# Kernel tuning notes

Hardware: AMD Instinct MI355X
Metric: run time of the kernel (lower is better)

Reference implementation:

```python
import jax, jax.numpy as jnp
import numpy as np

D_MODEL = 1024
N_HEADS = 16
HEAD_DIM = D_MODEL // N_HEADS
B, S = 2, 2048


def setup_inputs() -> dict:
    key = jax.random.key(0)
    ks = jax.random.split(key, 10)
    sd = 1.0 / np.sqrt(D_MODEL)
    return {
        "x": jax.random.normal(ks[0], (B, S, D_MODEL), dtype=jnp.float32),
        "mask": jnp.ones((1, 1, S, S), dtype=jnp.int32),
        "Wq": jax.random.normal(ks[1], (D_MODEL, D_MODEL), dtype=jnp.float32) * sd,
        "bq": jax.random.normal(ks[2], (D_MODEL,), dtype=jnp.float32) * sd,
        "Wk": jax.random.normal(ks[3], (D_MODEL, D_MODEL), dtype=jnp.float32) * sd,
        "bk": jax.random.normal(ks[4], (D_MODEL,), dtype=jnp.float32) * sd,
        "Wv": jax.random.normal(ks[5], (D_MODEL, D_MODEL), dtype=jnp.float32) * sd,
        "bv": jax.random.normal(ks[6], (D_MODEL,), dtype=jnp.float32) * sd,
        "Wo": jax.random.normal(ks[7], (D_MODEL, D_MODEL), dtype=jnp.float32) * sd,
        "bo": jax.random.normal(ks[8], (D_MODEL,), dtype=jnp.float32) * sd,
    }


def reference(x, mask, Wq, bq, Wk, bk, Wv, bv, Wo, bo):
    b, s, _ = x.shape
    scale = HEAD_DIM ** -0.5
    # projections (torch Linear: x @ W.T + b); split heads -> [b, h, s, d]
    def split_heads(t):
        return t.reshape(b, s, N_HEADS, HEAD_DIM).transpose(0, 2, 1, 3)
    q = split_heads(x @ Wq.T + bq)
    k = split_heads(x @ Wk.T + bk)
    v = split_heads(x @ Wv.T + bv)
    # scores: [b, h, s, s]
    scores = jnp.einsum("bhqd,bhkd->bhqk", q, k) * scale
    scores = jnp.where(mask == 0, jnp.float32(-1e20), scores)
    probs = jax.nn.softmax(scores, axis=-1)
    # dropout_rate = 0.0 (eval): identity
    ctx = jnp.einsum("bhqk,bhkd->bhqd", probs, v)
    ctx = ctx.transpose(0, 2, 1, 3).reshape(b, s, D_MODEL)
    return ctx @ Wo.T + bo
```

## Files before the change

### kernel.cpp

```cpp
#include <hip/hip_runtime.h>
#include <hip/hip_bf16.h>
#include <cstdint>
#include <cstddef>

#define D_MODEL 1024
#define NH      16
#define HD      64
#define BATCH   2
#define SEQ     2048
#define MTOT    (BATCH*SEQ)

typedef __bf16 bf16;
typedef __attribute__((ext_vector_type(8)))  __bf16 bf16x8;
typedef __attribute__((ext_vector_type(4)))  __bf16 bf16x4;
typedef __attribute__((ext_vector_type(2)))  __bf16 bf16x2;
typedef __attribute__((ext_vector_type(4)))  float  f32x4;
typedef __attribute__((ext_vector_type(16))) float  f32x16;
typedef __attribute__((ext_vector_type(2)))  unsigned int uint32x2;

__device__ __forceinline__ void gl_lds16(const void* g, void* l) {
    __builtin_amdgcn_global_load_lds(
        (const __attribute__((address_space(1))) uint32_t*)g,
        (__attribute__((address_space(3))) uint32_t*)l, 16, 0, 0);
}

__device__ __forceinline__ uint32_t pkbf(float a, float b) {
    union { bf16x2 v; uint32_t u; } t;
    t.v = (bf16x2){ (bf16)a, (bf16)b };
    return t.u;
}

__global__ __launch_bounds__(256)
void convert_all(const float* __restrict__ x,
                 const float* __restrict__ Wq, const float* __restrict__ Wk,
                 const float* __restrict__ Wv, const float* __restrict__ Wo,
                 bf16* __restrict__ xb,
                 bf16* __restrict__ Wqb, bf16* __restrict__ Wkb,
                 bf16* __restrict__ Wvb, bf16* __restrict__ Wob)
{
    const float* src; bf16* dst; size_t base = 0;
    int y = blockIdx.y;
    if      (y < 4)  { src = x;  dst = xb;  base = (size_t)y << 20; }
    else if (y == 4) { src = Wq; dst = Wqb; }
    else if (y == 5) { src = Wk; dst = Wkb; }
    else if (y == 6) { src = Wv; dst = Wvb; }
    else             { src = Wo; dst = Wob; }
    size_t i = base + ((size_t)blockIdx.x * 256 + threadIdx.x) * 4;
    float4 v = *(const float4*)(src + i);
    bf16x4 o = { (bf16)v.x, (bf16)v.y, (bf16)v.z, (bf16)v.w };
    *(bf16x4*)(dst + i) = o;
}

template<int MODE, int NTN>
__device__ __forceinline__ void gemm_body(const bf16* __restrict__ A,
                                          const bf16* __restrict__ W,
                                          const float* __restrict__ bias,
                                          void* __restrict__ OutV,
                                          float oscale, int mBase, int nBase,
                                          bf16* As, bf16* Bs)
{
    const int t      = threadIdx.x;
    const int l      = t & 63;
    const int w      = t >> 6;
    const int lane15 = l & 15;
    const int quad   = l >> 4;
    const int wm     = w >> 1;
    const int wn     = w & 1;
    const int WN     = NTN * 16;

    const int colsw = (((t & 7) ^ ((t >> 3) & 7))) * 16;
    const int sw    = lane15 & 7;

    const f32x4 vzero = {0.0f, 0.0f, 0.0f, 0.0f};
    f32x4 acc[4][NTN];
#pragma unroll
    for (int mt = 0; mt < 4; ++mt)
#pragma unroll
        for (int nt = 0; nt < NTN; ++nt) acc[mt][nt] = vzero;

    float bn_[NTN];
    float bm_[4][4];
    if (MODE == 3) {
#pragma unroll
        for (int mt = 0; mt < 4; ++mt)
#pragma unroll
            for (int r = 0; r < 4; ++r)
                bm_[mt][r] = bias[mBase + wm*64 + mt*16 + quad*4 + r];
    } else {
#pragma unroll
        for (int nt = 0; nt < NTN; ++nt)
            bn_[nt] = bias[nBase + wn*WN + nt*16 + lane15];
    }

    auto stage = [&](int kk, int buf) {
        char* Ad = (char*)As + buf * 16384;
        char* Bd = (char*)Bs + buf * (NTN * 4096);
#pragma unroll
        for (int c = 0; c < 4; ++c) {
            int row = (c*256 + t) >> 3;
            gl_lds16((const char*)A + (size_t)(mBase + row)*2048 + kk*2 + colsw,
                     Ad + (c*256 + w*64)*16);
        }
#pragma unroll
        for (int c = 0; c < NTN; ++c) {
            int row = (c*256 + t) >> 3;
            gl_lds16((const char*)W + (size_t)(nBase + row)*2048 + kk*2 + colsw,
                     Bd + (c*256 + w*64)*16);
        }
    };

    stage(0, 0);
    __syncthreads();
    stage(64, 1);

    for (int kt = 0; kt < 16; ++kt) {
        const int cb = kt & 1;
        const bf16* Ab = As + cb * 8192;
        const bf16* Bb = Bs + cb * (NTN * 2048);

#pragma unroll
        for (int kc = 0; kc < 2; ++kc) {
            bf16x8 af[4], bfr[NTN];
#pragma unroll
            for (int mt = 0; mt < 4; ++mt)
                af[mt] = *(const bf16x8*)(Ab + (wm*64 + mt*16 + lane15)*64
                                             + (((kc*4 + quad) ^ sw) * 8));
#pragma unroll
            for (int nt = 0; nt < NTN; ++nt)
                bfr[nt] = *(const bf16x8*)(Bb + (wn*WN + nt*16 + lane15)*64
                                              + (((kc*4 + quad) ^ sw) * 8));
#pragma unroll
            for (int mt = 0; mt < 4; ++mt)
#pragma unroll
                for (int nt = 0; nt < NTN; ++nt)
                    acc[mt][nt] = __builtin_amdgcn_mfma_f32_16x16x32_bf16(
                        af[mt], bfr[nt], acc[mt][nt], 0, 0, 0);
        }

        if (kt < 15) {
            __syncthreads();
            if (kt < 14) stage((kt + 2) * 64, cb);
        }
    }

#pragma unroll
    for (int mt = 0; mt < 4; ++mt) {
#pragma unroll
        for (int nt = 0; nt < NTN; ++nt) {
            int o = nBase + wn*WN + nt*16 + lane15;
#pragma unroll
            for (int r = 0; r < 4; ++r) {
                int m = mBase + wm*64 + mt*16 + quad*4 + r;
                if (MODE == 0) {
                    ((float*)OutV)[(size_t)m*D_MODEL + o] =
                        (acc[mt][nt][r] + bn_[nt]) * oscale;
                } else if (MODE == 1) {
                    int b = m >> 11, s = m & (SEQ-1);
                    int h = o >> 6,  dd = o & (HD-1);
                    ((bf16*)OutV)[(((size_t)(b*NH + h))*SEQ + s)*HD + dd] =
                        (bf16)((acc[mt][nt][r] + bn_[nt]) * oscale);
                } else {
                    int b = o >> 11, s = o & (SEQ-1);
                    int h = m >> 6,  dd = m & (HD-1);
                    ((bf16*)OutV)[(((size_t)(b*NH + h))*HD + dd)*SEQ + s] =
                        (bf16)((acc[mt][nt][r] + bm_[mt][r]) * oscale);
                }
            }
        }
    }
}

#define QSCALE (0.125f * 1.44269504088896f)

__global__ __launch_bounds__(256)
void gemm_qkv(const bf16* __restrict__ X,
              const bf16* __restrict__ Wq, const float* __restrict__ bq,
              const bf16* __restrict__ Wk, const float* __restrict__ bk,
              const bf16* __restrict__ Wv, const float* __restrict__ bv,
              bf16* __restrict__ Q, bf16* __restrict__ K, bf16* __restrict__ Vt)
{
    __shared__ __align__(16) bf16 As[2*128*64];
    __shared__ __align__(16) bf16 Bs[2*128*64];
    int lin = blockIdx.x + 8*blockIdx.y + 256*blockIdx.z;
    int wl  = (lin & 7)*96 + (lin >> 3);
    int bx = wl & 7, by = (wl >> 3) & 31, bz = wl >> 8;
    if (bz == 0)
        gemm_body<1,4>(X, Wq, bq, Q, QSCALE, by*128, bx*128, As, Bs);
    else if (bz == 1)
        gemm_body<1,4>(X, Wk, bk, K, 1.0f, by*128, bx*128, As, Bs);
    else
        gemm_body<3,4>(Wv, X, bv, Vt, 1.0f, bx*128, by*128, As, Bs);
}

__global__ __launch_bounds__(256)
void gemm_out(const bf16* __restrict__ A, const bf16* __restrict__ W,
              const float* __restrict__ b, float* __restrict__ O)
{
    __shared__ __align__(16) bf16 As[2*128*64];
    __shared__ __align__(16) bf16 Bs[2*64*64];
    int lin = blockIdx.x + 16*blockIdx.y;
    int wl  = (lin & 7)*64 + (lin >> 3);
    int bx = wl & 15, by = wl >> 4;
    gemm_body<0,2>(A, W, b, O, 1.0f, by*128, bx*64, As, Bs);
}

__device__ __forceinline__ float expsum(f32x16& s0, f32x16& s1) {
    float ps[4] = {0.f, 0.f, 0.f, 0.f};
#pragma unroll
    for (int e = 0; e < 16; ++e) {
        float p0 = __builtin_amdgcn_exp2f(s0[e]); s0[e] = p0;
        float p1 = __builtin_amdgcn_exp2f(s1[e]); s1[e] = p1;
        ps[e & 3] += p0 + p1;
    }
    return (ps[0] + ps[1]) + (ps[2] + ps[3]);
}

__device__ __forceinline__ void build_pf(const f32x16& s0, const f32x16& s1,
                                         bf16x8* pf) {
    uint32_t pp[8], pq[8];
#pragma unroll
    for (int i = 0; i < 8; ++i) {
        pp[i] = pkbf(s0[2*i], s0[2*i+1]);
        pq[i] = pkbf(s1[2*i], s1[2*i+1]);
    }
    union { uint32_t u[4]; bf16x8 f; } fr;
    uint32x2 r0, r1;
    r0 = __builtin_amdgcn_permlane32_swap(pp[0], pp[2], false, false);
    r1 = __builtin_amdgcn_permlane32_swap(pp[1], pp[3], false, false);
    fr.u[0] = r0[0]; fr.u[1] = r1[0]; fr.u[2] = r0[1]; fr.u[3] = r1[1];
    pf[0] = fr.f;
    r0 = __builtin_amdgcn_permlane32_swap(pp[4], pp[6], false, false);
    r1 = __builtin_amdgcn_permlane32_swap(pp[5], pp[7], false, false);
    fr.u[0] = r0[0]; fr.u[1] = r1[0]; fr.u[2] = r0[1]; fr.u[3] = r1[1];
    pf[1] = fr.f;
    r0 = __builtin_amdgcn_permlane32_swap(pq[0], pq[2], false, false);
    r1 = __builtin_amdgcn_permlane32_swap(pq[1], pq[3], false, false);
    fr.u[0] = r0[0]; fr.u[1] = r1[0]; fr.u[2] = r0[1]; fr.u[3] = r1[1];
    pf[2] = fr.f;
    r0 = __builtin_amdgcn_permlane32_swap(pq[4], pq[6], false, false);
    r1 = __builtin_amdgcn_permlane32_swap(pq[5], pq[7], false, false);
    fr.u[0] = r0[0]; fr.u[1] = r1[0]; fr.u[2] = r0[1]; fr.u[3] = r1[1];
    pf[3] = fr.f;
}

__global__ __launch_bounds__(512, 2)
void attn(const bf16* __restrict__ Qg, const bf16* __restrict__ Kg,
          const bf16* __restrict__ Vtg, bf16* __restrict__ ctx)
{
    __shared__ __align__(16) bf16 SMEM[2*16384];

    const int t      = threadIdx.x;
    const int w      = t >> 6;
    const int wg     = w >> 2;
    const int wq     = w & 3;
    const int l      = t & 63;
    const int lane31 = l & 31;
    const int half   = l >> 5;

    int lin = blockIdx.x + 8*blockIdx.y + 128*blockIdx.z;
    int wl  = (lin & 7)*32 + (lin >> 3);
    const int qt = wl & 7;
    const int h  = (wl >> 3) & 15;
    const int b  = wl >> 7;
    const size_t bh = (size_t)(b*NH + h);
    const bf16* Qb  = Qg  + bh*SEQ*HD;
    const bf16* Kb  = Kg  + bh*SEQ*HD;
    const bf16* Vtb = Vtg + bh*HD*SEQ;

    const int qA = qt*256 + wq*32 + lane31;

    bf16x8 qfA[4], qfB[4];
#pragma unroll
    for (int kc = 0; kc < 4; ++kc) {
        qfA[kc] = *(const bf16x8*)(Qb + (size_t)qA*HD + kc*16 + half*8);
        qfB[kc] = *(const bf16x8*)(Qb + (size_t)(qA+128)*HD + kc*16 + half*8);
    }

    const int lrow = l >> 3;
    const int csw  = ((l & 7) ^ lrow) * 8;

    auto issue = [&](int it, int buf) {
        const int kb = it * 128;
        bf16* Kbase = SMEM + buf*16384;
        bf16* Vbase = SMEM + buf*16384 + 8192;
#pragma unroll
        for (int seg = 0; seg < 2; ++seg) {
            int Rb = w*16 + seg*8;
            int R  = Rb + lrow;
            gl_lds16(Kb + (size_t)(kb + R)*HD + csw, Kbase + Rb*64);
            gl_lds16(Vtb + (size_t)(R & 63)*SEQ + kb + ((R >> 6) << 6) + csw,
                     Vbase + Rb*64);
        }
    };

    issue(0, 0);
    __syncthreads();
    issue(1, 1);

    float lA = 0.0f, lB = 0.0f;
    f32x16 oA0 = (f32x16)0.0f, oA1 = (f32x16)0.0f;
    f32x16 oB0 = (f32x16)0.0f, oB1 = (f32x16)0.0f;

    const int swl = lane31 & 7;
    const int NT2 = SEQ / 128;
    for (int kt = 0; kt < NT2; ++kt) {
        const int cb = kt & 1;
        const bf16* KsB = SMEM + cb*16384 + wg*64*64;
        const bf16* VsB = SMEM + cb*16384 + 8192 + wg*64*64;

        f32x16 sA0 = (f32x16)0.0f, sA1 = (f32x16)0.0f;
        f32x16 sB0 = (f32x16)0.0f, sB1 = (f32x16)0.0f;
#pragma unroll
        for (int kc = 0; kc < 4; ++kc) {
            const int co = ((kc*2 + half) ^ swl) * 8;
            bf16x8 k0 = *(const bf16x8*)(KsB + lane31*64      + co);
            bf16x8 k1 = *(const bf16x8*)(KsB + (32+lane31)*64 + co);
            sA0 = __builtin_amdgcn_mfma_f32_32x32x16_bf16(k0, qfA[kc], sA0, 0, 0, 0);
            sA1 = __builtin_amdgcn_mfma_f32_32x32x16_bf16(k1, qfA[kc], sA1, 0, 0, 0);
            sB0 = __builtin_amdgcn_mfma_f32_32x32x16_bf16(k0, qfB[kc], sB0, 0, 0, 0);
            sB1 = __builtin_amdgcn_mfma_f32_32x32x16_bf16(k1, qfB[kc], sB1, 0, 0, 0);
        }

        lA += expsum(sA0, sA1);
        bf16x8 pfA[4];
        build_pf(sA0, sA1, pfA);
        lB += expsum(sB0, sB1);
        bf16x8 pfB[4];
        build_pf(sB0, sB1, pfB);

#pragma unroll
        for (int kk = 0; kk < 4; ++kk) {
            const int co = ((kk*2 + half) ^ swl) * 8;
            bf16x8 v0 = *(const bf16x8*)(VsB + lane31*64      + co);
            bf16x8 v1 = *(const bf16x8*)(VsB + (32+lane31)*64 + co);
            oA0 = __builtin_amdgcn_mfma_f32_32x32x16_bf16(v0, pfA[kk], oA0, 0, 0, 0);
            oA1 = __builtin_amdgcn_mfma_f32_32x32x16_bf16(v1, pfA[kk], oA1, 0, 0, 0);
            oB0 = __builtin_amdgcn_mfma_f32_32x32x16_bf16(v0, pfB[kk], oB0, 0, 0, 0);
            oB1 = __builtin_amdgcn_mfma_f32_32x32x16_bf16(v1, pfB[kk], oB1, 0, 0, 0);
        }

        if (kt < NT2-1) {
            __syncthreads();
            if (kt + 2 < NT2) issue(kt + 2, cb);
        }
    }

    {
        union { float f; uint32_t u; } c; c.f = lA;
        uint32x2 r = __builtin_amdgcn_permlane32_swap(c.u, c.u, false, false);
        union { uint32_t u; float f; } x0, x1; x0.u = r[0]; x1.u = r[1];
        lA = x0.f + x1.f;
        c.f = lB;
        r = __builtin_amdgcn_permlane32_swap(c.u, c.u, false, false);
        x0.u = r[0]; x1.u = r[1];
        lB = x0.f + x1.f;
    }

    __syncthreads();
    float* sc = (float*)SMEM;
    const int sidx = (wq*64 + l)*36;
    if (wg == 1) {
        *(f32x4*)(sc + sidx +  0) = (f32x4){oA0[0],oA0[1],oA0[2],oA0[3]};
        *(f32x4*)(sc + sidx +  4) = (f32x4){oA0[4],oA0[5],oA0[6],oA0[7]};
        *(f32x4*)(sc + sidx +  8) = (f32x4){oA0[8],oA0[9],oA0[10],oA0[11]};
        *(f32x4*)(sc + sidx + 12) = (f32x4){oA0[12],oA0[13],oA0[14],oA0[15]};
        *(f32x4*)(sc + sidx + 16) = (f32x4){oA1[0],oA1[1],oA1[2],oA1[3]};
        *(f32x4*)(sc + sidx + 20) = (f32x4){oA1[4],oA1[5],oA1[6],oA1[7]};
        *(f32x4*)(sc + sidx + 24) = (f32x4){oA1[8],oA1[9],oA1[10],oA1[11]};
        *(f32x4*)(sc + sidx + 28) = (f32x4){oA1[12],oA1[13],oA1[14],oA1[15]};
        sc[sidx + 32] = lA;
    }
    __syncthreads();
    if (wg == 0) {
#pragma unroll
        for (int e = 0; e < 16; ++e) {
            oA0[e] += sc[sidx + e];
            oA1[e] += sc[sidx + 16 + e];
        }
        lA += sc[sidx + 32];
        float inv = 1.0f / lA;
        size_t base = (size_t)(b*SEQ + qA)*D_MODEL + h*HD;
#pragma unroll
        for (int rg = 0; rg < 4; ++rg) {
            int d0 = rg*8 + half*4;
            bf16x4 a0 = { (bf16)(oA0[rg*4+0]*inv), (bf16)(oA0[rg*4+1]*inv),
                          (bf16)(oA0[rg*4+2]*inv), (bf16)(oA0[rg*4+3]*inv) };
            *(bf16x4*)(ctx + base + d0) = a0;
            bf16x4 a1 = { (bf16)(oA1[rg*4+0]*inv), (bf16)(oA1[rg*4+1]*inv),
                          (bf16)(oA1[rg*4+2]*inv), (bf16)(oA1[rg*4+3]*inv) };
            *(bf16x4*)(ctx + base + 32 + d0) = a1;
        }
    }
    __syncthreads();
    if (wg == 1) {
        *(f32x4*)(sc + sidx +  0) = (f32x4){oB0[0],oB0[1],oB0[2],oB0[3]};
        *(f32x4*)(sc + sidx +  4) = (f32x4){oB0[4],oB0[5],oB0[6],oB0[7]};
        *(f32x4*)(sc + sidx +  8) = (f32x4){oB0[8],oB0[9],oB0[10],oB0[11]};
        *(f32x4*)(sc + sidx + 12) = (f32x4){oB0[12],oB0[13],oB0[14],oB0[15]};
        *(f32x4*)(sc + sidx + 16) = (f32x4){oB1[0],oB1[1],oB1[2],oB1[3]};
        *(f32x4*)(sc + sidx + 20) = (f32x4){oB1[4],oB1[5],oB1[6],oB1[7]};
        *(f32x4*)(sc + sidx + 24) = (f32x4){oB1[8],oB1[9],oB1[10],oB1[11]};
        *(f32x4*)(sc + sidx + 28) = (f32x4){oB1[12],oB1[13],oB1[14],oB1[15]};
        sc[sidx + 32] = lB;
    }
    __syncthreads();
    if (wg == 0) {
#pragma unroll
        for (int e = 0; e < 16; ++e) {
            oB0[e] += sc[sidx + e];
            oB1[e] += sc[sidx + 16 + e];
        }
        lB += sc[sidx + 32];
        float inv = 1.0f / lB;
        size_t base = (size_t)(b*SEQ + qA + 128)*D_MODEL + h*HD;
#pragma unroll
        for (int rg = 0; rg < 4; ++rg) {
            int d0 = rg*8 + half*4;
            bf16x4 a0 = { (bf16)(oB0[rg*4+0]*inv), (bf16)(oB0[rg*4+1]*inv),
                          (bf16)(oB0[rg*4+2]*inv), (bf16)(oB0[rg*4+3]*inv) };
            *(bf16x4*)(ctx + base + d0) = a0;
            bf16x4 a1 = { (bf16)(oB1[rg*4+0]*inv), (bf16)(oB1[rg*4+1]*inv),
                          (bf16)(oB1[rg*4+2]*inv), (bf16)(oB1[rg*4+3]*inv) };
            *(bf16x4*)(ctx + base + 32 + d0) = a1;
        }
    }
}

extern "C" void kernel_launch(void* const* d_in, const int* in_sizes, int n_in,
                              void* d_out, int out_size, void* d_ws, size_t ws_size,
                              hipStream_t stream)
{
    const float* x  = (const float*)d_in[0];
    const float* Wq = (const float*)d_in[2];
    const float* bq = (const float*)d_in[3];
    const float* Wk = (const float*)d_in[4];
    const float* bk = (const float*)d_in[5];
    const float* Wv = (const float*)d_in[6];
    const float* bv = (const float*)d_in[7];
    const float* Wo = (const float*)d_in[8];
    const float* bo = (const float*)d_in[9];
    float* out = (float*)d_out;

    char* ws = (char*)d_ws;
    const size_t MB = (size_t)1024*1024;
    bf16* xb  = (bf16*)(ws);
    bf16* Wqb = (bf16*)(ws +  8*MB);
    bf16* Wkb = (bf16*)(ws + 10*MB);
    bf16* Wvb = (bf16*)(ws + 12*MB);
    bf16* Wob = (bf16*)(ws + 14*MB);
    bf16* Q   = (bf16*)(ws + 16*MB);
    bf16* K   = (bf16*)(ws + 24*MB);
    bf16* Vt  = (bf16*)(ws + 32*MB);
    bf16* ctx = (bf16*)(ws + 40*MB);

    convert_all<<<dim3(1024, 8), 256, 0, stream>>>(x, Wq, Wk, Wv, Wo,
                                                   xb, Wqb, Wkb, Wvb, Wob);
    gemm_qkv<<<dim3(8, 32, 3), 256, 0, stream>>>(xb, Wqb, bq, Wkb, bk, Wvb, bv, Q, K, Vt);
    attn<<<dim3(8, 16, 2), 512, 0, stream>>>(Q, K, Vt, ctx);
    gemm_out<<<dim3(16, 32, 1), 256, 0, stream>>>(ctx, Wob, bo, out);
}
```

Baseline: 187.7 us.

## Interleave B-half exp2 with A-half PV MFMAs and raise MFMA priority

Restructures the attention inner loop so the exponentials for the second query sub-tile are computed inside the first sub-tile's P·V MFMA loop, overlapping transcendental VALU work with matrix-core work. V fragments are hoisted out of the loop and loaded once into registers, then reused by both sub-tiles. MFMA sections are wrapped in s_setprio to favour matrix-issue waves. This raises register pressure (extra V fragment arrays) under launch bounds of 512 threads with 2 blocks, which risks spills or reduced occupancy.

```diff
diff --git a/kernel.cpp b/kernel.cpp
--- a/kernel.cpp
+++ b/kernel.cpp
@@ -243,6 +243,8 @@
     pf[3] = fr.f;
 }
 
+#define MFMA32(a, b, c) __builtin_amdgcn_mfma_f32_32x32x16_bf16(a, b, c, 0, 0, 0)
+
 __global__ __launch_bounds__(512, 2)
 void attn(const bf16* __restrict__ Qg, const bf16* __restrict__ Kg,
           const bf16* __restrict__ Vtg, bf16* __restrict__ ctx)
@@ -310,34 +312,56 @@
 
         f32x16 sA0 = (f32x16)0.0f, sA1 = (f32x16)0.0f;
         f32x16 sB0 = (f32x16)0.0f, sB1 = (f32x16)0.0f;
+        __builtin_amdgcn_s_setprio(1);
 #pragma unroll
         for (int kc = 0; kc < 4; ++kc) {
             const int co = ((kc*2 + half) ^ swl) * 8;
             bf16x8 k0 = *(const bf16x8*)(KsB + lane31*64      + co);
             bf16x8 k1 = *(const bf16x8*)(KsB + (32+lane31)*64 + co);
-            sA0 = __builtin_amdgcn_mfma_f32_32x32x16_bf16(k0, qfA[kc], sA0, 0, 0, 0);
-            sA1 = __builtin_amdgcn_mfma_f32_32x32x16_bf16(k1, qfA[kc], sA1, 0, 0, 0);
-            sB0 = __builtin_amdgcn_mfma_f32_32x32x16_bf16(k0, qfB[kc], sB0, 0, 0, 0);
-            sB1 = __builtin_amdgcn_mfma_f32_32x32x16_bf16(k1, qfB[kc], sB1, 0, 0, 0);
+            sA0 = MFMA32(k0, qfA[kc], sA0);
+            sA1 = MFMA32(k1, qfA[kc], sA1);
+            sB0 = MFMA32(k0, qfB[kc], sB0);
+            sB1 = MFMA32(k1, qfB[kc], sB1);
+        }
+        __builtin_amdgcn_s_setprio(0);
+
+        bf16x8 vf0[4], vf1[4];
+#pragma unroll
+        for (int kk = 0; kk < 4; ++kk) {
+            const int co = ((kk*2 + half) ^ swl) * 8;
+            vf0[kk] = *(const bf16x8*)(VsB + lane31*64      + co);
+            vf1[kk] = *(const bf16x8*)(VsB + (32+lane31)*64 + co);
         }
 
         lA += expsum(sA0, sA1);
         bf16x8 pfA[4];
         build_pf(sA0, sA1, pfA);
-        lB += expsum(sB0, sB1);
+
+        float psB[4] = {0.f, 0.f, 0.f, 0.f};
+        __builtin_amdgcn_s_setprio(1);
+#pragma unroll
+        for (int kk = 0; kk < 4; ++kk) {
+            oA0 = MFMA32(vf0[kk], pfA[kk], oA0);
+            oA1 = MFMA32(vf1[kk], pfA[kk], oA1);
+#pragma unroll
+            for (int e = kk*4; e < kk*4 + 4; ++e) {
+                float p0 = __builtin_amdgcn_exp2f(sB0[e]); sB0[e] = p0;
+                float p1 = __builtin_amdgcn_exp2f(sB1[e]); sB1[e] = p1;
+                psB[e & 3] += p0 + p1;
+            }
+        }
+        __builtin_amdgcn_s_setprio(0);
+        lB += (psB[0] + psB[1]) + (psB[2] + psB[3]);
         bf16x8 pfB[4];
         build_pf(sB0, sB1, pfB);
 
+        __builtin_amdgcn_s_setprio(1);
 #pragma unroll
         for (int kk = 0; kk < 4; ++kk) {
-            const int co = ((kk*2 + half) ^ swl) * 8;
-            bf16x8 v0 = *(const bf16x8*)(VsB + lane31*64      + co);
-            bf16x8 v1 = *(const bf16x8*)(VsB + (32+lane31)*64 + co);
-            oA0 = __builtin_amdgcn_mfma_f32_32x32x16_bf16(v0, pfA[kk], oA0, 0, 0, 0);
-            oA1 = __builtin_amdgcn_mfma_f32_32x32x16_bf16(v1, pfA[kk], oA1, 0, 0, 0);
-            oB0 = __builtin_amdgcn_mfma_f32_32x32x16_bf16(v0, pfB[kk], oB0, 0, 0, 0);
-            oB1 = __builtin_amdgcn_mfma_f32_32x32x16_bf16(v1, pfB[kk], oB1, 0, 0, 0);
-        }
+            oB0 = MFMA32(vf0[kk], pfB[kk], oB0);
+            oB1 = MFMA32(vf1[kk], pfB[kk], oB1);
+        }
+        __builtin_amdgcn_s_setprio(0);
 
         if (kt < NT2-1) {
             __syncthreads();
```

Result: slower. 207.6 us (+10.6%).
